# Kernel tuning notes

Hardware: AMD Instinct MI355X
Metric: run time of the kernel (lower is better)

The kernel has to match this reference:

```python
import jax, jax.numpy as jnp
import numpy as np

B, H, W, D, C, NH = 2, 32, 32, 32, 256, 8
LN_EPS = 1e-3  # keras LayerNormalization default epsilon


def _ln(x, g, b):
    m = jnp.mean(x, axis=-1, keepdims=True)
    v = jnp.mean(jnp.square(x - m), axis=-1, keepdims=True)
    return (x - m) * jax.lax.rsqrt(v + LN_EPS) * g + b


def setup_inputs() -> dict:
    key = jax.random.key(0)
    ks = jax.random.split(key, 8)
    w = lambda k, shape, fan: (jax.random.normal(k, shape, jnp.float32) / np.sqrt(fan)).astype(jnp.float32)
    return {
        "q": jax.random.normal(ks[0], (B, H, W, D, C), jnp.float32),
        "kv": jax.random.normal(ks[1], (B, H, W, D, C), jnp.float32),
        "wq_w": w(ks[2], (C, C), C), "wq_b": jnp.zeros((C,), jnp.float32),
        "wk_w": w(ks[3], (C, C), C), "wk_b": jnp.zeros((C,), jnp.float32),
        "wv_w": w(ks[4], (C, C), C), "wv_b": jnp.zeros((C,), jnp.float32),
        "ln1_g": jnp.ones((C,), jnp.float32), "ln1_b": jnp.zeros((C,), jnp.float32),
        "ff1_w": w(ks[5], (C, 4 * C), C), "ff1_b": jnp.zeros((4 * C,), jnp.float32),
        "ff2_w": w(ks[6], (4 * C, C), 4 * C), "ff2_b": jnp.zeros((C,), jnp.float32),
        "ln2_g": jnp.ones((C,), jnp.float32), "ln2_b": jnp.zeros((C,), jnp.float32),
    }


def reference(q, kv, wq_w, wq_b, wk_w, wk_b, wv_w, wv_b,
              ln1_g, ln1_b, ff1_w, ff1_b, ff2_w, ff2_b, ln2_g, ln2_b):
    Bq, Hh, Ww, Dd, Cc = q.shape
    dh = Cc // NH
    qf = q.reshape(Bq, -1, Cc)          # (B, N, C), N = H*W*D
    inq = qf
    kvf = kv.reshape(Bq, -1, Cc)

    def split_heads(x):                  # (B, N, C) -> (B, h, N, dh)
        return x.reshape(Bq, -1, NH, dh).transpose(0, 2, 1, 3)

    qh = split_heads(qf @ wq_w + wq_b)
    kh = split_heads(kvf @ wk_w + wk_b)
    vh = split_heads(kvf @ wv_w + wv_b)

    # efficient (linear) attention: softmax over N on k^T, softmax over dh on q
    k_norm = jax.nn.softmax(kh.transpose(0, 1, 3, 2), axis=-1)   # (B, h, dh, N)
    q_norm = jax.nn.softmax(qh, axis=-1)                         # (B, h, N, dh)
    context = jnp.einsum('bhdn,bhne->bhde', k_norm, vh)          # (B, h, dh, dh)
    attn = jnp.einsum('bhnd,bhde->bhne', q_norm, context)        # (B, h, N, dh)
    attn = attn.transpose(0, 2, 1, 3).reshape(Bq, -1, Cc)

    x = _ln(inq + attn, ln1_g, ln1_b)
    ff = jax.nn.gelu(x @ ff1_w + ff1_b, approximate=False) @ ff2_w + ff2_b
    out = _ln(x + ff, ln2_g, ln2_b)
    return out.reshape(Bq, Hh, Ww, Dd, Cc)
```

## Files before the change

kernel.cpp:

```cpp
#include <hip/hip_runtime.h>
#include <hip/hip_bf16.h>

#define NTOK_B   32768
#define TOK_TOT  65536
#define CDIM     256
#define NHEAD    8
#define DHEAD    32
#define FFDIM    1024
#define LN_EPS   1e-3f

typedef __attribute__((ext_vector_type(8))) short bf16x8;
typedef __attribute__((ext_vector_type(4))) float f32x4;

__device__ __forceinline__ float bf2f(short s) {
    union { unsigned u; float f; } v; v.u = ((unsigned)(unsigned short)s) << 16; return v.f;
}
__device__ __forceinline__ short f2bf(float f) {
    union { float f; unsigned u; } v; v.f = f;
    unsigned r = (v.u + 0x7FFFu + ((v.u >> 16) & 1u)) >> 16;
    return (short)r;
}

__device__ __forceinline__ void gld_lds16(const void* g, void* l) {
    __builtin_amdgcn_global_load_lds(
        (const __attribute__((address_space(1))) unsigned int*)g,
        (__attribute__((address_space(3))) unsigned int*)l, 16, 0, 0);
}

__global__ __launch_bounds__(256) void cast_bf16(const float* __restrict__ in,
                                                 short* __restrict__ out)
{
    long i = ((long)blockIdx.x * 256 + threadIdx.x) * 8;
    float4 a = *(const float4*)(in + i);
    float4 b = *(const float4*)(in + i + 4);
    short t[8];
    t[0] = f2bf(a.x); t[1] = f2bf(a.y); t[2] = f2bf(a.z); t[3] = f2bf(a.w);
    t[4] = f2bf(b.x); t[5] = f2bf(b.y); t[6] = f2bf(b.z); t[7] = f2bf(b.w);
    *(int4*)(out + i) = *(const int4*)t;
}

__global__ __launch_bounds__(256) void transpose_k(const float* __restrict__ in,
                                                   short* __restrict__ out, int K, int N)
{
    __shared__ float t[32][33];
    int kt = blockIdx.x * 32, nt = blockIdx.y * 32;
    int tx = threadIdx.x, ty = threadIdx.y;
#pragma unroll
    for (int i = 0; i < 4; ++i)
        t[ty + i * 8][tx] = in[(long)(kt + ty + i * 8) * N + nt + tx];
    __syncthreads();
#pragma unroll
    for (int i = 0; i < 4; ++i)
        out[(long)(nt + ty + i * 8) * K + kt + tx] = f2bf(t[tx][ty + i * 8]);
}

__global__ __launch_bounds__(256) void concat_bias(const float* __restrict__ a,
                                                   const float* __restrict__ b,
                                                   float* __restrict__ o)
{
    int i = blockIdx.x * 256 + threadIdx.x;
    o[i] = (i < 256) ? a[i] : b[i - 256];
}

template<int ACT, int OF32, int NBX>
__global__ __launch_bounds__(256) void gemm_bt(const short* __restrict__ Xv,
                                               const short* __restrict__ Wt,
                                               const float* __restrict__ bias,
                                               void* __restrict__ Outv,
                                               int N, int K, int ldx, int ldo)
{
    constexpr int LOG2NBX = (NBX == 2) ? 1 : (NBX == 4) ? 2 : 3;
    __shared__ __align__(16) short As[3][4096];
    __shared__ __align__(16) short Bs[3][4096];

    const int tid  = threadIdx.x;
    const int lane = tid & 63;
    const int wave = tid >> 6;
    const int wm   = (wave >> 1) * 4;
    const int wn   = (wave & 1) * 4;

    const int bid  = blockIdx.x;
    const int xcd  = bid & 7;
    const int j    = bid >> 3;
    const int nblk = j & (NBX - 1);
    const int mblk = xcd * 64 + (j >> LOG2NBX);
    const long m0  = (long)mblk * 128;
    const int  n0  = nblk * 128;

    f32x4 acc[4][4];
#pragma unroll
    for (int i = 0; i < 4; ++i)
#pragma unroll
        for (int jj = 0; jj < 4; ++jj) acc[i][jj] = (f32x4)0.0f;

    const int NT = K >> 5;

    auto stage = [&](int kt, int buf) {
#pragma unroll
        for (int p = 0; p < 2; ++p) {
            int idx = tid + p * 256;
            int row = (idx >> 6) * 16 + (idx & 15);
            int qq  = (idx >> 4) & 3;
            int lofs = (p * 256 + wave * 64) * 8;
            gld_lds16(Xv + (m0 + row) * (long)ldx + kt * 32 + qq * 8, As[buf] + lofs);
            gld_lds16(Wt + (long)(n0 + row) * K + kt * 32 + qq * 8,  Bs[buf] + lofs);
        }
    };

    stage(0, 0);
    if (NT > 1) stage(1, 1);
    int cb = 0;
    for (int kt = 0; kt < NT; ++kt) {
        __builtin_amdgcn_sched_barrier(0);
        if (kt + 1 < NT) asm volatile("s_waitcnt vmcnt(4)" ::: "memory");
        else             asm volatile("s_waitcnt vmcnt(0)" ::: "memory");
        __builtin_amdgcn_s_barrier();
        __builtin_amdgcn_sched_barrier(0);
        if (kt + 2 < NT) {
            int sb = cb + 2; if (sb >= 3) sb -= 3;
            stage(kt + 2, sb);
        }
        bf16x8 a[4], b[4];
#pragma unroll
        for (int i = 0; i < 4; ++i) a[i] = *(const bf16x8*)(As[cb] + ((wm + i) * 64 + lane) * 8);
#pragma unroll
        for (int jj = 0; jj < 4; ++jj) b[jj] = *(const bf16x8*)(Bs[cb] + ((wn + jj) * 64 + lane) * 8);
#pragma unroll
        for (int i = 0; i < 4; ++i)
#pragma unroll
            for (int jj = 0; jj < 4; ++jj)
                acc[i][jj] = __builtin_amdgcn_mfma_f32_16x16x32_bf16(a[i], b[jj], acc[i][jj], 0, 0, 0);
        cb = (cb + 1 == 3) ? 0 : cb + 1;
    }

    const int crow0 = (wave >> 1) * 64 + (lane >> 4) * 4;
    const int ccol0 = (wave & 1) * 64 + (lane & 15);
#pragma unroll
    for (int jj = 0; jj < 4; ++jj) {
        int col = n0 + ccol0 + jj * 16;
        float bb = bias[col];
#pragma unroll
        for (int i = 0; i < 4; ++i) {
            long row = m0 + crow0 + i * 16;
#pragma unroll
            for (int r = 0; r < 4; ++r) {
                float v = acc[i][jj][r] + bb;
                if (ACT == 1) {
                    float w = -1.5957691216057308f * (v + 0.044715f * v * v * v);
                    v = v / (1.0f + __expf(w));
                }
                if constexpr (OF32) ((float*)Outv)[(row + r) * (long)ldo + col] = v;
                else                ((short*)Outv)[(row + r) * (long)ldo + col] = f2bf(v);
            }
        }
    }
}

#define CCH 512
#define CPS 64
__global__ __launch_bounds__(256) void context_k(const short* __restrict__ QKV,
                                                 float* __restrict__ ctx,
                                                 float* __restrict__ ksum)
{
    const int b = blockIdx.z, h = blockIdx.y;
    const long tokbase = (long)b * NTOK_B + (long)blockIdx.x * CCH;
    __shared__ __align__(16) float kb[2][CPS][32];
    __shared__ __align__(16) float vb[2][CPS][32];
    const int tid  = threadIdx.x;
    const int wave = tid >> 6;
    const int lane = tid & 63;
    const int t    = lane;
    const int koff = (wave < 2) ? 256 : 512;
    const int choff = (wave & 1) * 16;
    const short* src0 = QKV + (tokbase + t) * 768 + koff + h * 32 + choff;

    const int d2 = lane >> 2;
    const int eg = lane & 3;
    __align__(16) float acc[2][8];
#pragma unroll
    for (int i = 0; i < 2; ++i)
#pragma unroll
        for (int j = 0; j < 8; ++j) acc[i][j] = 0.0f;
    float s0 = 0.0f, s1 = 0.0f;

    int4 p0 = *(const int4*)src0;
    int4 p1 = *(const int4*)(src0 + 8);
    const int NP = CCH / CPS;
    for (int p = 0; p < NP; ++p) {
        int4 n0 = p0, n1 = p1;
        if (p + 1 < NP) {
            const short* sn = src0 + (long)(p + 1) * CPS * 768;
            n0 = *(const int4*)sn;
            n1 = *(const int4*)(sn + 8);
        }
        {
            short sh[16];
            *(int4*)&sh[0] = p0; *(int4*)&sh[8] = p1;
            float v[16];
            if (wave < 2) {
#pragma unroll
                for (int i = 0; i < 16; ++i) v[i] = __expf(bf2f(sh[i]));
            } else {
#pragma unroll
                for (int i = 0; i < 16; ++i) v[i] = bf2f(sh[i]);
            }
            char* rowp = (char*)((wave < 2) ? &kb[p & 1][t][0] : &vb[p & 1][t][0]);
            int sw = (t & 7) << 4;
#pragma unroll
            for (int q = 0; q < 4; ++q) {
                int qq = (choff >> 2) + q;
                *(float4*)(rowp + ((qq * 16) ^ sw)) =
                    make_float4(v[q * 4], v[q * 4 + 1], v[q * 4 + 2], v[q * 4 + 3]);
            }
        }
        __syncthreads();
        {
            const int buf = p & 1;
#pragma unroll
            for (int k = 0; k < 16; ++k) {
                int tt = wave * 16 + k;
                int sw = (tt & 7) << 4;
                const char* krow = (const char*)&kb[buf][tt][0];
                const char* vrow = (const char*)&vb[buf][tt][0];
                float2 kd = *(const float2*)(krow + ((d2 * 8) ^ sw));
                float4 va = *(const float4*)(vrow + ((eg * 32) ^ sw));
                float4 vbb = *(const float4*)(vrow + ((eg * 32 + 16) ^ sw));
                acc[0][0] += kd.x * va.x;  acc[0][1] += kd.x * va.y;
                acc[0][2] += kd.x * va.z;  acc[0][3] += kd.x * va.w;
                acc[0][4] += kd.x * vbb.x; acc[0][5] += kd.x * vbb.y;
                acc[0][6] += kd.x * vbb.z; acc[0][7] += kd.x * vbb.w;
                acc[1][0] += kd.y * va.x;  acc[1][1] += kd.y * va.y;
                acc[1][2] += kd.y * va.z;  acc[1][3] += kd.y * va.w;
                acc[1][4] += kd.y * vbb.x; acc[1][5] += kd.y * vbb.y;
                acc[1][6] += kd.y * vbb.z; acc[1][7] += kd.y * vbb.w;
                if (eg == 0) { s0 += kd.x; s1 += kd.y; }
            }
        }
        p0 = n0; p1 = n1;
    }

    __syncthreads();
    float* red = &kb[0][0][0];
    float* rs  = &vb[0][0][0];
#pragma unroll
    for (int dd = 0; dd < 2; ++dd) {
        *(float4*)&red[wave * 1024 + (d2 * 2 + dd) * 32 + eg * 8]     = *(float4*)&acc[dd][0];
        *(float4*)&red[wave * 1024 + (d2 * 2 + dd) * 32 + eg * 8 + 4] = *(float4*)&acc[dd][4];
    }
    if (eg == 0) { rs[wave * 32 + d2 * 2] = s0; rs[wave * 32 + d2 * 2 + 1] = s1; }
    __syncthreads();
    {
        float* cbase = ctx + ((long)(b * 8 + h) * 32) * 32;
        int i0 = tid * 4;
        float4 a  = *(float4*)&red[i0];
        float4 b4 = *(float4*)&red[1024 + i0];
        float4 c4 = *(float4*)&red[2048 + i0];
        float4 d4 = *(float4*)&red[3072 + i0];
        atomicAdd(cbase + i0 + 0, a.x + b4.x + c4.x + d4.x);
        atomicAdd(cbase + i0 + 1, a.y + b4.y + c4.y + d4.y);
        atomicAdd(cbase + i0 + 2, a.z + b4.z + c4.z + d4.z);
        atomicAdd(cbase + i0 + 3, a.w + b4.w + c4.w + d4.w);
        if (tid < 32) {
            float s = rs[tid] + rs[32 + tid] + rs[64 + tid] + rs[96 + tid];
            atomicAdd(ksum + b * 256 + h * 32 + tid, s);
        }
    }
}

__global__ __launch_bounds__(256) void attn_ln1(const short* __restrict__ QKV,
                                                const float* __restrict__ qin,
                                                const float* __restrict__ ctx,
                                                const float* __restrict__ ksum,
                                                const float* __restrict__ g1,
                                                const float* __restrict__ b1,
                                                short* __restrict__ xout)
{
    long tok0blk = (long)blockIdx.x * 128;
    int b = (int)(tok0blk >> 15);
    __shared__ __align__(16) float qn[16][292];
    __shared__ __align__(16) float xb[16][292];
    __shared__ float red[16][8][2];
    __shared__ float mr[16][2];
    int tid = threadIdx.x;
    int h = tid >> 5, e = tid & 31;

    float cregs[32];
    {
        const float* cp = ctx + ((long)(b * 8 + h) * 32) * 32 + e;
        const float* zs = ksum + b * 256 + h * 32;
#pragma unroll
        for (int d = 0; d < 32; ++d) cregs[d] = cp[d * 32] / zs[d];
    }

    for (int sub = 0; sub < 8; ++sub) {
        long tok0 = tok0blk + sub * 16;
        if (tid < 128) {
            int tA = tid >> 3, hA = tid & 7;
            const short* Qp = QKV + (tok0 + tA) * 768 + hA * 32;
            short qv[32];
            *(int4*)&qv[0]  = *(const int4*)(Qp);
            *(int4*)&qv[8]  = *(const int4*)(Qp + 8);
            *(int4*)&qv[16] = *(const int4*)(Qp + 16);
            *(int4*)&qv[24] = *(const int4*)(Qp + 24);
            float f[32]; float mx = -1e30f;
#pragma unroll
            for (int i = 0; i < 32; ++i) { f[i] = bf2f(qv[i]); mx = fmaxf(mx, f[i]); }
            float s = 0.0f;
#pragma unroll
            for (int i = 0; i < 32; ++i) { f[i] = __expf(f[i] - mx); s += f[i]; }
            float inv = 1.0f / s;
            float* qrow = &qn[tA][hA * 36];
#pragma unroll
            for (int i = 0; i < 32; ++i) qrow[i] = f[i] * inv;
        }
        __syncthreads();
        {
            int cch = h * 32 + e;
#pragma unroll 2
            for (int t = 0; t < 16; ++t) {
                const float4* qr = (const float4*)&qn[t][h * 36];
                float a = 0.0f;
#pragma unroll
                for (int d4 = 0; d4 < 8; ++d4) {
                    float4 qv = qr[d4];
                    a += qv.x * cregs[d4 * 4 + 0] + qv.y * cregs[d4 * 4 + 1]
                       + qv.z * cregs[d4 * 4 + 2] + qv.w * cregs[d4 * 4 + 3];
                }
                float iv = qin[(tok0 + t) * 256 + cch];
                xb[t][cch] = a + iv;
            }
        }
        __syncthreads();
        if (tid < 128) {
            int tC = tid & 15, sC = tid >> 4;
            float s = 0, ss = 0;
            const float* xr = &xb[tC][sC * 32];
#pragma unroll
            for (int i = 0; i < 32; ++i) { float v = xr[i]; s += v; ss += v * v; }
            red[tC][sC][0] = s; red[tC][sC][1] = ss;
        }
        __syncthreads();
        if (tid < 16) {
            float s = 0, ss = 0;
#pragma unroll
            for (int k = 0; k < 8; ++k) { s += red[tid][k][0]; ss += red[tid][k][1]; }
            float mean = s * (1.0f / 256.0f);
            float var  = ss * (1.0f / 256.0f) - mean * mean;
            mr[tid][0] = mean; mr[tid][1] = rsqrtf(var + LN_EPS);
        }
        __syncthreads();
        if (tid < 128) {
            int tC = tid & 15, sC = tid >> 4;
            float mean = mr[tC][0], rstd = mr[tC][1];
            const float* xr = &xb[tC][sC * 32];
            short ov[32];
#pragma unroll
            for (int i = 0; i < 32; ++i) {
                int c = sC * 32 + i;
                float v = (xr[i] - mean) * rstd * g1[c] + b1[c];
                ov[i] = f2bf(v);
            }
            int4* op = (int4*)(xout + (tok0 + tC) * 256 + sC * 32);
            op[0] = *(int4*)&ov[0];  op[1] = *(int4*)&ov[8];
            op[2] = *(int4*)&ov[16]; op[3] = *(int4*)&ov[24];
        }
        __syncthreads();
    }
}

__global__ __launch_bounds__(256) void ln2_k(const short* __restrict__ xbuf,
                                             float* __restrict__ out,
                                             const float* __restrict__ g2,
                                             const float* __restrict__ b2)
{
    int wave = threadIdx.x >> 6, lane = threadIdx.x & 63;
    long tok = (long)blockIdx.x * 4 + wave;
    int c0 = lane * 4;
    const short* xp = xbuf + tok * 256 + c0;
    float* yp = out + tok * 256 + c0;
    short xv[4];
    *(int2*)xv = *(const int2*)xp;
    float4 yv = *(const float4*)yp;
    float v[4]; float s = 0, ss = 0;
    v[0] = bf2f(xv[0]) + yv.x; v[1] = bf2f(xv[1]) + yv.y;
    v[2] = bf2f(xv[2]) + yv.z; v[3] = bf2f(xv[3]) + yv.w;
#pragma unroll
    for (int i = 0; i < 4; ++i) { s += v[i]; ss += v[i] * v[i]; }
#pragma unroll
    for (int off = 32; off > 0; off >>= 1) { s += __shfl_xor(s, off); ss += __shfl_xor(ss, off); }
    float mean = s * (1.0f / 256.0f);
    float rstd = rsqrtf(ss * (1.0f / 256.0f) - mean * mean + LN_EPS);
    float4 ov;
    ov.x = (v[0] - mean) * rstd * g2[c0 + 0] + b2[c0 + 0];
    ov.y = (v[1] - mean) * rstd * g2[c0 + 1] + b2[c0 + 1];
    ov.z = (v[2] - mean) * rstd * g2[c0 + 2] + b2[c0 + 2];
    ov.w = (v[3] - mean) * rstd * g2[c0 + 3] + b2[c0 + 3];
    *(float4*)yp = ov;
}

extern "C" void kernel_launch(void* const* d_in, const int* in_sizes, int n_in,
                              void* d_out, int out_size, void* d_ws, size_t ws_size,
                              hipStream_t stream)
{
    const float* q    = (const float*)d_in[0];
    const float* kv   = (const float*)d_in[1];
    const float* wq_w = (const float*)d_in[2];
    const float* wq_b = (const float*)d_in[3];
    const float* wk_w = (const float*)d_in[4];
    const float* wk_b = (const float*)d_in[5];
    const float* wv_w = (const float*)d_in[6];
    const float* wv_b = (const float*)d_in[7];
    const float* ln1g = (const float*)d_in[8];
    const float* ln1b = (const float*)d_in[9];
    const float* ff1w = (const float*)d_in[10];
    const float* ff1b = (const float*)d_in[11];
    const float* ff2w = (const float*)d_in[12];
    const float* ff2b = (const float*)d_in[13];
    const float* ln2g = (const float*)d_in[14];
    const float* ln2b = (const float*)d_in[15];

    char* w = (char*)d_ws;
    short* Wtq = (short*)w; w += 131072;
    short* Wtk = (short*)w; w += 131072;
    short* Wtv = (short*)w; w += 131072;
    short* Wt1 = (short*)w; w += 524288;
    short* Wt2 = (short*)w; w += 524288;
    float* ksm = (float*)w; w += 2048;
    float* bkv = (float*)w; w += 2048;
    float* ctx = (float*)w; w += 65536;
    short* xbuf= (short*)w; w += 33554432;
    short* QKV = (short*)w; w += 134217728;
    short* kvb = (short*)w; w += 33554432;
    short* h1  = QKV;
    short* qb  = xbuf;
    float* y   = (float*)d_out;

    cast_bf16<<<8192, 256, 0, stream>>>(q,  qb);
    cast_bf16<<<8192, 256, 0, stream>>>(kv, kvb);

    dim3 tb(32, 8);
    transpose_k<<<dim3(8, 8),  tb, 0, stream>>>(wq_w, Wtq, 256, 256);
    transpose_k<<<dim3(8, 8),  tb, 0, stream>>>(wk_w, Wtk, 256, 256);
    transpose_k<<<dim3(8, 8),  tb, 0, stream>>>(wv_w, Wtv, 256, 256);
    transpose_k<<<dim3(8, 32), tb, 0, stream>>>(ff1w, Wt1, 256, 1024);
    transpose_k<<<dim3(32, 8), tb, 0, stream>>>(ff2w, Wt2, 1024, 256);
    concat_bias<<<2, 256, 0, stream>>>(wk_b, wv_b, bkv);

    gemm_bt<0,0,2><<<1024, 256, 0, stream>>>(qb,  Wtq, wq_b, QKV + 0,   256, 256, 256, 768);
    gemm_bt<0,0,4><<<2048, 256, 0, stream>>>(kvb, Wtk, bkv,  QKV + 256, 512, 256, 256, 768);

    hipMemsetAsync(ctx, 0, 65536, stream);
    hipMemsetAsync(ksm, 0, 2048, stream);
    context_k<<<dim3(NTOK_B / CCH, 8, 2), 256, 0, stream>>>(QKV, ctx, ksm);

    attn_ln1<<<512, 256, 0, stream>>>(QKV, q, ctx, ksm, ln1g, ln1b, xbuf);

    gemm_bt<1,0,8><<<4096, 256, 0, stream>>>(xbuf, Wt1, ff1b, h1, 1024, 256, 256, 1024);
    gemm_bt<0,1,2><<<1024, 256, 0, stream>>>(h1,  Wt2, ff2b, y,  256, 1024, 1024, 256);

    ln2_k<<<16384, 256, 0, stream>>>(xbuf, y, ln2g, ln2b);
}
```

Measured before the change: 590.5 us.

## Fuse FF2 GEMM with residual LayerNorm and stage GEMM epilogue through LDS

Replaces the FF2 GEMM plus separate ln2 kernel with one kernel where each block computes a 64x256 output tile covering full rows, so residual add and LayerNorm happen in registers before a single fp32 store. This removes the fp32 y write and read round trip and one launch. The bf16 GEMM epilogue now stages results through padded LDS so each global store is a coalesced 16-byte write instead of scattered 2-byte stores. The fused kernel uses 60KB of LDS and 64-row tiles, which may lower occupancy and per-block reuse of the FF2 weights.

```diff
diff --git a/kernel.cpp b/kernel.cpp
--- a/kernel.cpp
+++ b/kernel.cpp
@@ -62,16 +62,17 @@
     o[i] = (i < 256) ? a[i] : b[i - 256];
 }
 
-template<int ACT, int OF32, int NBX>
+template<int ACT, int NBX>
 __global__ __launch_bounds__(256) void gemm_bt(const short* __restrict__ Xv,
                                                const short* __restrict__ Wt,
                                                const float* __restrict__ bias,
-                                               void* __restrict__ Outv,
+                                               short* __restrict__ Outp,
                                                int N, int K, int ldx, int ldo)
 {
     constexpr int LOG2NBX = (NBX == 2) ? 1 : (NBX == 4) ? 2 : 3;
-    __shared__ __align__(16) short As[3][4096];
-    __shared__ __align__(16) short Bs[3][4096];
+    __shared__ __align__(16) char smem[49152];
+    short* As = (short*)smem;
+    short* Bs = (short*)(smem + 24576);
 
     const int tid  = threadIdx.x;
     const int lane = tid & 63;
@@ -101,9 +102,9 @@
             int idx = tid + p * 256;
             int row = (idx >> 6) * 16 + (idx & 15);
             int qq  = (idx >> 4) & 3;
-            int lofs = (p * 256 + wave * 64) * 8;
-            gld_lds16(Xv + (m0 + row) * (long)ldx + kt * 32 + qq * 8, As[buf] + lofs);
-            gld_lds16(Wt + (long)(n0 + row) * K + kt * 32 + qq * 8,  Bs[buf] + lofs);
+            int lofs = buf * 4096 + (p * 256 + wave * 64) * 8;
+            gld_lds16(Xv + (m0 + row) * (long)ldx + kt * 32 + qq * 8, As + lofs);
+            gld_lds16(Wt + (long)(n0 + row) * K + kt * 32 + qq * 8,  Bs + lofs);
         }
     };
 
@@ -122,9 +123,9 @@
         }
         bf16x8 a[4], b[4];
 #pragma unroll
-        for (int i = 0; i < 4; ++i) a[i] = *(const bf16x8*)(As[cb] + ((wm + i) * 64 + lane) * 8);
-#pragma unroll
-        for (int jj = 0; jj < 4; ++jj) b[jj] = *(const bf16x8*)(Bs[cb] + ((wn + jj) * 64 + lane) * 8);
+        for (int i = 0; i < 4; ++i) a[i] = *(const bf16x8*)(As + cb * 4096 + ((wm + i) * 64 + lane) * 8);
+#pragma unroll
+        for (int jj = 0; jj < 4; ++jj) b[jj] = *(const bf16x8*)(Bs + cb * 4096 + ((wn + jj) * 64 + lane) * 8);
 #pragma unroll
         for (int i = 0; i < 4; ++i)
 #pragma unroll
@@ -133,15 +134,16 @@
         cb = (cb + 1 == 3) ? 0 : cb + 1;
     }
 
+    __syncthreads();
+    short* Cs = (short*)smem;
     const int crow0 = (wave >> 1) * 64 + (lane >> 4) * 4;
     const int ccol0 = (wave & 1) * 64 + (lane & 15);
 #pragma unroll
     for (int jj = 0; jj < 4; ++jj) {
-        int col = n0 + ccol0 + jj * 16;
-        float bb = bias[col];
+        int colw = ccol0 + jj * 16;
+        float bb = bias[n0 + colw];
 #pragma unroll
         for (int i = 0; i < 4; ++i) {
-            long row = m0 + crow0 + i * 16;
 #pragma unroll
             for (int r = 0; r < 4; ++r) {
                 float v = acc[i][jj][r] + bb;
@@ -149,8 +151,147 @@
                     float w = -1.5957691216057308f * (v + 0.044715f * v * v * v);
                     v = v / (1.0f + __expf(w));
                 }
-                if constexpr (OF32) ((float*)Outv)[(row + r) * (long)ldo + col] = v;
-                else                ((short*)Outv)[(row + r) * (long)ldo + col] = f2bf(v);
+                Cs[(crow0 + i * 16 + r) * 136 + colw] = f2bf(v);
+            }
+        }
+    }
+    __syncthreads();
+#pragma unroll
+    for (int it = 0; it < 8; ++it) {
+        int ch = tid + it * 256;
+        int row = ch >> 4, c8 = ch & 15;
+        int4 v = *(const int4*)(Cs + row * 136 + c8 * 8);
+        *(int4*)(Outp + (m0 + row) * (long)ldo + n0 + c8 * 8) = v;
+    }
+}
+
+__global__ __launch_bounds__(256) void ff2_ln(const short* __restrict__ H,
+                                              const short* __restrict__ Wt2,
+                                              const float* __restrict__ b2f,
+                                              const short* __restrict__ xbuf,
+                                              const float* __restrict__ g2,
+                                              const float* __restrict__ b2,
+                                              float* __restrict__ y)
+{
+    __shared__ __align__(16) char smem[61440];
+
+    const int tid  = threadIdx.x;
+    const int lane = tid & 63;
+    const int wave = tid >> 6;
+
+    const int bid  = blockIdx.x;
+    const int mblk = (bid & 7) * 128 + (bid >> 3);
+    const long m0  = (long)mblk * 64;
+
+    f32x4 acc[4][4];
+#pragma unroll
+    for (int i = 0; i < 4; ++i)
+#pragma unroll
+        for (int jj = 0; jj < 4; ++jj) acc[i][jj] = (f32x4)0.0f;
+
+    auto stage = [&](int kt, int buf) {
+        char* base = smem + buf * 20480;
+        {
+            int row = wave * 16 + (lane & 15);
+            int qq  = lane >> 4;
+            gld_lds16(H + (m0 + row) * 1024L + kt * 32 + qq * 8,
+                      base + wave * 1024);
+        }
+#pragma unroll
+        for (int p = 0; p < 4; ++p) {
+            int ti  = p * 4 + wave;
+            int row = ti * 16 + (lane & 15);
+            int qq  = lane >> 4;
+            gld_lds16(Wt2 + row * 1024L + kt * 32 + qq * 8,
+                      base + 4096 + (p * 256 + wave * 64) * 16);
+        }
+    };
+
+    const int NT = 32;
+    stage(0, 0);
+    stage(1, 1);
+    int cb = 0;
+    for (int kt = 0; kt < NT; ++kt) {
+        __builtin_amdgcn_sched_barrier(0);
+        if (kt + 1 < NT) asm volatile("s_waitcnt vmcnt(5)" ::: "memory");
+        else             asm volatile("s_waitcnt vmcnt(0)" ::: "memory");
+        __builtin_amdgcn_s_barrier();
+        __builtin_amdgcn_sched_barrier(0);
+        if (kt + 2 < NT) {
+            int sb = cb + 2; if (sb >= 3) sb -= 3;
+            stage(kt + 2, sb);
+        }
+        const short* Ab = (const short*)(smem + cb * 20480);
+        const short* Bb = (const short*)(smem + cb * 20480 + 4096);
+        bf16x8 a[4], b[4];
+#pragma unroll
+        for (int i = 0; i < 4; ++i) a[i] = *(const bf16x8*)(Ab + (i * 64 + lane) * 8);
+#pragma unroll
+        for (int jj = 0; jj < 4; ++jj) b[jj] = *(const bf16x8*)(Bb + ((wave * 4 + jj) * 64 + lane) * 8);
+#pragma unroll
+        for (int i = 0; i < 4; ++i)
+#pragma unroll
+            for (int jj = 0; jj < 4; ++jj)
+                acc[i][jj] = __builtin_amdgcn_mfma_f32_16x16x32_bf16(a[i], b[jj], acc[i][jj], 0, 0, 0);
+        cb = (cb + 1 == 3) ? 0 : cb + 1;
+    }
+
+    __syncthreads();
+    float* red = (float*)smem;
+    float* mr  = red + 512;
+
+    float g2c[4], b2c[4], bfc[4];
+#pragma unroll
+    for (int jj = 0; jj < 4; ++jj) {
+        int col = wave * 64 + (lane & 15) + jj * 16;
+        bfc[jj] = b2f[col]; g2c[jj] = g2[col]; b2c[jj] = b2[col];
+    }
+
+#pragma unroll
+    for (int i = 0; i < 4; ++i) {
+#pragma unroll
+        for (int r = 0; r < 4; ++r) {
+            int row = i * 16 + (lane >> 4) * 4 + r;
+            float s = 0.0f, ss = 0.0f;
+#pragma unroll
+            for (int jj = 0; jj < 4; ++jj) {
+                int col = wave * 64 + (lane & 15) + jj * 16;
+                float val = acc[i][jj][r] + bfc[jj]
+                          + bf2f(xbuf[(m0 + row) * 256 + col]);
+                acc[i][jj][r] = val;
+                s += val; ss += val * val;
+            }
+            s  += __shfl_xor(s, 1);  ss += __shfl_xor(ss, 1);
+            s  += __shfl_xor(s, 2);  ss += __shfl_xor(ss, 2);
+            s  += __shfl_xor(s, 4);  ss += __shfl_xor(ss, 4);
+            s  += __shfl_xor(s, 8);  ss += __shfl_xor(ss, 8);
+            if ((lane & 15) == 0) {
+                red[(row * 4 + wave) * 2]     = s;
+                red[(row * 4 + wave) * 2 + 1] = ss;
+            }
+        }
+    }
+    __syncthreads();
+    if (tid < 64) {
+        float s  = red[tid * 8] + red[tid * 8 + 2] + red[tid * 8 + 4] + red[tid * 8 + 6];
+        float ss = red[tid * 8 + 1] + red[tid * 8 + 3] + red[tid * 8 + 5] + red[tid * 8 + 7];
+        float mean = s * (1.0f / 256.0f);
+        float var  = ss * (1.0f / 256.0f) - mean * mean;
+        mr[tid * 2]     = mean;
+        mr[tid * 2 + 1] = rsqrtf(var + LN_EPS);
+    }
+    __syncthreads();
+#pragma unroll
+    for (int i = 0; i < 4; ++i) {
+#pragma unroll
+        for (int r = 0; r < 4; ++r) {
+            int row = i * 16 + (lane >> 4) * 4 + r;
+            float mean = mr[row * 2], rstd = mr[row * 2 + 1];
+#pragma unroll
+            for (int jj = 0; jj < 4; ++jj) {
+                int col = wave * 64 + (lane & 15) + jj * 16;
+                y[(m0 + row) * 256 + col] =
+                    (acc[i][jj][r] - mean) * rstd * g2c[jj] + b2c[jj];
             }
         }
     }
@@ -368,36 +509,6 @@
     }
 }
 
-__global__ __launch_bounds__(256) void ln2_k(const short* __restrict__ xbuf,
-                                             float* __restrict__ out,
-                                             const float* __restrict__ g2,
-                                             const float* __restrict__ b2)
-{
-    int wave = threadIdx.x >> 6, lane = threadIdx.x & 63;
-    long tok = (long)blockIdx.x * 4 + wave;
-    int c0 = lane * 4;
-    const short* xp = xbuf + tok * 256 + c0;
-    float* yp = out + tok * 256 + c0;
-    short xv[4];
-    *(int2*)xv = *(const int2*)xp;
-    float4 yv = *(const float4*)yp;
-    float v[4]; float s = 0, ss = 0;
-    v[0] = bf2f(xv[0]) + yv.x; v[1] = bf2f(xv[1]) + yv.y;
-    v[2] = bf2f(xv[2]) + yv.z; v[3] = bf2f(xv[3]) + yv.w;
-#pragma unroll
-    for (int i = 0; i < 4; ++i) { s += v[i]; ss += v[i] * v[i]; }
-#pragma unroll
-    for (int off = 32; off > 0; off >>= 1) { s += __shfl_xor(s, off); ss += __shfl_xor(ss, off); }
-    float mean = s * (1.0f / 256.0f);
-    float rstd = rsqrtf(ss * (1.0f / 256.0f) - mean * mean + LN_EPS);
-    float4 ov;
-    ov.x = (v[0] - mean) * rstd * g2[c0 + 0] + b2[c0 + 0];
-    ov.y = (v[1] - mean) * rstd * g2[c0 + 1] + b2[c0 + 1];
-    ov.z = (v[2] - mean) * rstd * g2[c0 + 2] + b2[c0 + 2];
-    ov.w = (v[3] - mean) * rstd * g2[c0 + 3] + b2[c0 + 3];
-    *(float4*)yp = ov;
-}
-
 extern "C" void kernel_launch(void* const* d_in, const int* in_sizes, int n_in,
                               void* d_out, int out_size, void* d_ws, size_t ws_size,
                               hipStream_t stream)
@@ -446,8 +557,8 @@
     transpose_k<<<dim3(32, 8), tb, 0, stream>>>(ff2w, Wt2, 1024, 256);
     concat_bias<<<2, 256, 0, stream>>>(wk_b, wv_b, bkv);
 
-    gemm_bt<0,0,2><<<1024, 256, 0, stream>>>(qb,  Wtq, wq_b, QKV + 0,   256, 256, 256, 768);
-    gemm_bt<0,0,4><<<2048, 256, 0, stream>>>(kvb, Wtk, bkv,  QKV + 256, 512, 256, 256, 768);
+    gemm_bt<0,2><<<1024, 256, 0, stream>>>(qb,  Wtq, wq_b, QKV + 0,   256, 256, 256, 768);
+    gemm_bt<0,4><<<2048, 256, 0, stream>>>(kvb, Wtk, bkv,  QKV + 256, 512, 256, 256, 768);
 
     hipMemsetAsync(ctx, 0, 65536, stream);
     hipMemsetAsync(ksm, 0, 2048, stream);
@@ -455,8 +566,7 @@
 
     attn_ln1<<<512, 256, 0, stream>>>(QKV, q, ctx, ksm, ln1g, ln1b, xbuf);
 
-    gemm_bt<1,0,8><<<4096, 256, 0, stream>>>(xbuf, Wt1, ff1b, h1, 1024, 256, 256, 1024);
-    gemm_bt<0,1,2><<<1024, 256, 0, stream>>>(h1,  Wt2, ff2b, y,  256, 1024, 1024, 256);
-
-    ln2_k<<<16384, 256, 0, stream>>>(xbuf, y, ln2g, ln2b);
-}
+    gemm_bt<1,8><<<4096, 256, 0, stream>>>(xbuf, Wt1, ff1b, h1, 1024, 256, 256, 1024);
+
+    ff2_ln<<<1024, 256, 0, stream>>>(h1, Wt2, ff2b, xbuf, ln2g, ln2b, y);
+}
```

After: 570.5 us. 1.04x faster.
